# Optimization experiments

Hardware: AMD Instinct MI355X
Metric: run time of the kernel (lower is better)

## Reference

```python
import jax, jax.numpy as jnp
import numpy as np

DIM = 512          # must equal heads*dim_head for LayerNorm(dim) on q/k to be valid
SCALE = 64 ** -0.5  # dim_head ** -0.5
EPS = 1e-5


def layer_norm(x, g, b):
    mu = jnp.mean(x, axis=-1, keepdims=True)
    var = jnp.var(x, axis=-1, keepdims=True)
    return (x - mu) * jax.lax.rsqrt(var + EPS) * g + b


def setup_inputs() -> dict:
    key = jax.random.key(0)
    ks = jax.random.split(key, 8)
    b, n, m, d = 4, 4096, 4096, DIM
    x = jax.random.normal(ks[0], (b, n, d), dtype=jnp.float32)
    context = jax.random.normal(ks[1], (b, m, d), dtype=jnp.float32)
    s = 1.0 / np.sqrt(d)
    Wq = jax.random.normal(ks[2], (d, d), dtype=jnp.float32) * s
    Wkv = jax.random.normal(ks[3], (d, 2 * d), dtype=jnp.float32) * s
    Wo = jax.random.normal(ks[4], (d, d), dtype=jnp.float32) * s
    bo = jnp.zeros((d,), dtype=jnp.float32)
    ln_g = jnp.ones((d,), dtype=jnp.float32)
    ln_b = jnp.zeros((d,), dtype=jnp.float32)
    return {"x": x, "context": context, "Wq": Wq, "Wkv": Wkv, "Wo": Wo,
            "bo": bo, "ln_g": ln_g, "ln_b": ln_b}


def reference(x, context, Wq, Wkv, Wo, bo, ln_g, ln_b):
    # linear projections (no bias on q/kv, matching nn.Linear(bias=False))
    q = x @ Wq                                   # [b, n, d]
    kv = context @ Wkv                           # [b, m, 2d]
    k, v = jnp.split(kv, 2, axis=-1)             # [b, m, d] each
    # qk-norm: same LayerNorm params applied to q and k
    q = layer_norm(q, ln_g, ln_b)
    k = layer_norm(k, ln_g, ln_b)
    # NOTE: the original never splits heads -> full-dim single-head attention
    dots = jnp.einsum('bnd,bmd->bnm', q, k) * SCALE  # [b, n, m]
    attn = jax.nn.softmax(dots, axis=-1)
    out = jnp.einsum('bnm,bmd->bnd', attn, v)        # [b, n, d]
    return out @ Wo + bo
```

## Files before the change

kernel.cpp:

```cpp
#include <hip/hip_runtime.h>

typedef __bf16 bf16_t;
typedef bf16_t bf16x8 __attribute__((ext_vector_type(8)));
typedef float f32x4 __attribute__((ext_vector_type(4)));
typedef float f32x16 __attribute__((ext_vector_type(16)));

#define DIMD 512
#define NSEQ 4096
#define BATCH 4
#define ROWS (BATCH * NSEQ)
#define MPART 2
#define FIXMAX 20.0f

__device__ __forceinline__ void gload_lds16(const bf16_t* g, bf16_t* l) {
    __builtin_amdgcn_global_load_lds((const __attribute__((address_space(1))) unsigned int*)g,
                                     (__attribute__((address_space(3))) unsigned int*)l,
                                     16, 0, 0);
}

__device__ __forceinline__ int packbf(float lo, float hi) {
    union { bf16_t h[2]; int w; } u;
    u.h[0] = (bf16_t)lo;
    u.h[1] = (bf16_t)hi;
    return u.w;
}

__global__ void detect_mode(const unsigned* __restrict__ g, int* __restrict__ mode) {
    if (threadIdx.x == 0) *mode = (*g == 0x3F800000u) ? 1 : 0;
}

__global__ __launch_bounds__(256) void transpose_w(const void* __restrict__ in,
                                                   bf16_t* __restrict__ out,
                                                   int R, int C,
                                                   const int* __restrict__ modep) {
    int mode = *modep;
    int idx = blockIdx.x * 256 + threadIdx.x;
    if (idx < R * C) {
        int r = idx / C;
        int c = idx - r * C;
        float v = mode ? ((const float*)in)[idx] : (float)((const bf16_t*)in)[idx];
        out[c * R + r] = (bf16_t)v;
    }
}

__global__ void convert_vec(const void* __restrict__ in, bf16_t* __restrict__ out,
                            int n, const int* __restrict__ modep) {
    int mode = *modep;
    int i = blockIdx.x * 256 + threadIdx.x;
    if (i < n)
        out[i] = mode ? (bf16_t)((const float*)in)[i] : ((const bf16_t*)in)[i];
}

__global__ __launch_bounds__(256) void ln_rows(bf16_t* __restrict__ buf,
                                               const bf16_t* __restrict__ g,
                                               const bf16_t* __restrict__ bvec,
                                               float mult, int swz) {
    int w = threadIdx.x >> 6;
    int lane = threadIdx.x & 63;
    int row = blockIdx.x * 4 + w;
    const bf16_t* p = buf + (size_t)row * 512 + lane * 8;
    bf16x8 xv = *(const bf16x8*)p;
    float x[8];
    float s = 0.f, sq = 0.f;
#pragma unroll
    for (int i = 0; i < 8; ++i) {
        x[i] = (float)xv[i];
        s += x[i];
        sq += x[i] * x[i];
    }
#pragma unroll
    for (int off = 1; off < 64; off <<= 1) {
        s += __shfl_xor(s, off, 64);
        sq += __shfl_xor(sq, off, 64);
    }
    float mean = s * (1.0f / 512.0f);
    float var = fmaxf(sq * (1.0f / 512.0f) - mean * mean, 0.0f);
    float rstd = rsqrtf(var + 1e-5f);
    bf16x8 gv = *(const bf16x8*)(g + lane * 8);
    bf16x8 bv = *(const bf16x8*)(bvec + lane * 8);
    bf16x8 o;
#pragma unroll
    for (int i = 0; i < 8; ++i)
        o[i] = (bf16_t)(((x[i] - mean) * rstd * (float)gv[i] + (float)bv[i]) * mult);
    int outlane = swz ? (lane ^ (row & 7)) : lane;
    *(bf16x8*)(buf + (size_t)row * 512 + outlane * 8) = o;
}

template <int EPI>
__global__ __launch_bounds__(256) void gemm_nt(const void* __restrict__ A,
                                               const bf16_t* __restrict__ Bt,
                                               void* __restrict__ Cout,
                                               bf16_t* __restrict__ C2,
                                               int K, int ldc,
                                               const bf16_t* __restrict__ bias,
                                               const int* __restrict__ amodep,
                                               const int* __restrict__ omodep,
                                               const float* __restrict__ mlp) {
    __shared__ bf16_t As[128 * 32];
    __shared__ bf16_t Bs[128 * 32];
    int amode = (EPI != 2 && amodep) ? *amodep : 0;
    int t = threadIdx.x;
    int w = t >> 6;
    int lane = t & 63;
    int r16 = lane & 15;
    int quad = lane >> 4;
    int m0 = blockIdx.x * 128;
    int n0 = blockIdx.y * 128;
    int wr = w >> 1, wc = w & 1;

    f32x4 acc[4][4];
#pragma unroll
    for (int m = 0; m < 4; ++m)
#pragma unroll
        for (int n = 0; n < 4; ++n) acc[m][n] = f32x4{0.f, 0.f, 0.f, 0.f};

    int brow = w * 32 + (lane >> 2);
    int bswz = ((lane & 3) ^ ((brow >> 1) & 3)) * 8;
    const bf16_t* bsrc0 = Bt + (size_t)(n0 + brow) * K + bswz;
    const bf16_t* bsrc1 = bsrc0 + (size_t)16 * K;
    bf16_t* bdst0 = Bs + (w * 32) * 32;
    bf16_t* bdst1 = Bs + (w * 32 + 16) * 32;

    int a_r = t >> 1;
    int kh = (t & 1) * 16;
    int aswz = (a_r >> 1) & 3;
    bf16_t* adst0 = As + a_r * 32 + (((t & 1) * 2 + 0) ^ aswz) * 8;
    bf16_t* adst1 = As + a_r * 32 + (((t & 1) * 2 + 1) ^ aswz) * 8;

    float combine_scl = 0.f;
    if (EPI == 2)
        combine_scl = 1.0f / (mlp[m0 + a_r] + mlp[ROWS + m0 + a_r]);

    const bf16_t* abase = As + (wr * 64 + r16) * 32 + (quad ^ ((r16 >> 1) & 3)) * 8;
    const bf16_t* bbase = Bs + (wc * 64 + r16) * 32 + (quad ^ ((r16 >> 1) & 3)) * 8;

    for (int kt = 0; kt < K; kt += 32) {
        bf16x8 av0, av1;
        if (EPI == 2) {
            const bf16_t* r0 = (const bf16_t*)A + (size_t)(m0 + a_r) * 512 + kt + kh;
            const bf16_t* r1 = r0 + (size_t)ROWS * 512;
            bf16x8 x0 = *(const bf16x8*)r0;
            bf16x8 x1 = *(const bf16x8*)(r0 + 8);
            bf16x8 y0 = *(const bf16x8*)r1;
            bf16x8 y1 = *(const bf16x8*)(r1 + 8);
#pragma unroll
            for (int j = 0; j < 8; ++j) {
                av0[j] = (bf16_t)(((float)x0[j] + (float)y0[j]) * combine_scl);
                av1[j] = (bf16_t)(((float)x1[j] + (float)y1[j]) * combine_scl);
            }
        } else if (amode) {
            const float* Af = (const float*)A + (size_t)(m0 + a_r) * K + kt + kh;
            f32x4 f0 = *(const f32x4*)(Af + 0);
            f32x4 f1 = *(const f32x4*)(Af + 4);
            f32x4 f2 = *(const f32x4*)(Af + 8);
            f32x4 f3 = *(const f32x4*)(Af + 12);
#pragma unroll
            for (int j = 0; j < 4; ++j) {
                av0[j] = (bf16_t)f0[j];
                av0[j + 4] = (bf16_t)f1[j];
                av1[j] = (bf16_t)f2[j];
                av1[j + 4] = (bf16_t)f3[j];
            }
        } else {
            const bf16_t* Ab = (const bf16_t*)A + (size_t)(m0 + a_r) * K + kt + kh;
            av0 = *(const bf16x8*)Ab;
            av1 = *(const bf16x8*)(Ab + 8);
        }
        *(bf16x8*)adst0 = av0;
        *(bf16x8*)adst1 = av1;
        gload_lds16(bsrc0 + kt, bdst0);
        gload_lds16(bsrc1 + kt, bdst1);
        __syncthreads();

        bf16x8 af[4], bfr[4];
#pragma unroll
        for (int m = 0; m < 4; ++m) af[m] = *(const bf16x8*)(abase + m * 16 * 32);
#pragma unroll
        for (int n = 0; n < 4; ++n) bfr[n] = *(const bf16x8*)(bbase + n * 16 * 32);
        __builtin_amdgcn_s_setprio(1);
#pragma unroll
        for (int m = 0; m < 4; ++m)
#pragma unroll
            for (int n = 0; n < 4; ++n)
                acc[m][n] = __builtin_amdgcn_mfma_f32_16x16x32_bf16(af[m], bfr[n], acc[m][n], 0, 0, 0);
        __builtin_amdgcn_s_setprio(0);
        __syncthreads();
    }

    int omode = (EPI == 2 && omodep) ? *omodep : 0;
#pragma unroll
    for (int n = 0; n < 4; ++n) {
        int col = n0 + wc * 64 + n * 16 + r16;
        float bv = (EPI == 2 && bias) ? (float)bias[col] : 0.0f;
#pragma unroll
        for (int m = 0; m < 4; ++m) {
#pragma unroll
            for (int r = 0; r < 4; ++r) {
                int row = m0 + wr * 64 + m * 16 + quad * 4 + r;
                float val = acc[m][n][r] + bv;
                if (EPI == 0) {
                    ((bf16_t*)Cout)[(size_t)row * ldc + col] = (bf16_t)val;
                } else if (EPI == 1) {
                    if (col < 512) {
                        ((bf16_t*)Cout)[(size_t)row * 512 + col] = (bf16_t)val;
                    } else {
                        int d = col - 512;
                        C2[(size_t)(row >> 5) * 16384 + (d >> 3) * 256 + ((row & 31) >> 3) * 64
                           + (d & 7) * 8 + (row & 7)] = (bf16_t)val;
                    }
                } else {
                    if (omode)
                        ((float*)Cout)[(size_t)row * 512 + col] = val;
                    else
                        ((bf16_t*)Cout)[(size_t)row * 512 + col] = (bf16_t)val;
                }
            }
        }
    }
}

__global__ __launch_bounds__(512, 2) void flash_attn(const bf16_t* __restrict__ q,
                                                     const bf16_t* __restrict__ kn,
                                                     const bf16_t* __restrict__ vt,
                                                     bf16_t* __restrict__ Opart,
                                                     float* __restrict__ ml) {
    __shared__ bf16_t Ks[2][32 * 512];
    __shared__ bf16_t Vs[2][32 * 512];
    __shared__ float Pd[8][4][64][4];

    int t = threadIdx.x;
    int w = t >> 6;
    int lane = t & 63;
    int l31 = lane & 31;
    int h = lane >> 5;
    int qb = w & 3;
    int dh = w >> 2;
    int part = blockIdx.y;
    int qrow0 = blockIdx.x * 128 + qb * 32;
    int bb = (blockIdx.x * 128) >> 12;
    int krow0 = bb * NSEQ + part * (NSEQ / MPART);
    const int niter = (NSEQ / MPART) / 32;

    bf16x8 qf[16];
    {
        const bf16_t* qp = q + (size_t)(qrow0 + l31) * 512 + dh * 256 + h * 8;
#pragma unroll
        for (int ks = 0; ks < 16; ++ks) qf[ks] = *(const bf16x8*)(qp + ks * 16);
    }

    f32x16 O[8];
#pragma unroll
    for (int i = 0; i < 8; ++i)
#pragma unroll
        for (int j = 0; j < 16; ++j) O[i][j] = 0.f;
    float lsum = 0.f;
    int swz7 = l31 & 7;

    const bf16_t* KbA[2] = {&Ks[0][l31 * 512], &Ks[1][l31 * 512]};
    int voff = dh * 8192 + (l31 >> 3) * 256 + (l31 & 7) * 8 + h * 64;
    const bf16_t* VbA[2] = {&Vs[0][voff], &Vs[1][voff]};

#define STAGE(mt, bufi)                                                                          \
    {                                                                                            \
        if (w < 4) {                                                                             \
            const bf16_t* ksrc_ = kn + (size_t)(krow0 + (mt) + w * 8) * 512 + lane * 8;          \
            bf16_t* kd_ = &Ks[bufi][(w * 8) * 512];                                              \
            _Pragma("unroll")                                                                    \
            for (int i_ = 0; i_ < 8; ++i_)                                                       \
                gload_lds16(ksrc_ + i_ * 512, kd_ + i_ * 512);                                   \
        } else {                                                                                 \
            const bf16_t* vsrc_ = vt + (size_t)((krow0 + (mt)) >> 5) * 16384                     \
                                  + (size_t)((w - 4) * 8) * 512 + lane * 8;                      \
            bf16_t* vd_ = &Vs[bufi][((w - 4) * 8) * 512];                                        \
            _Pragma("unroll")                                                                    \
            for (int i_ = 0; i_ < 8; ++i_)                                                       \
                gload_lds16(vsrc_ + i_ * 512, vd_ + i_ * 512);                                   \
        }                                                                                        \
    }

#define FLASH_BODY(it, bufi)                                                                      \
    {                                                                                             \
        __syncthreads();                                                                          \
        if ((it) + 1 < niter) STAGE(((it) + 1) * 32, ((it) + 1) & 1);                             \
        f32x16 a;                                                                                 \
        _Pragma("unroll") for (int j = 0; j < 16; ++j) a[j] = 0.f;                                \
        __builtin_amdgcn_s_setprio(1);                                                            \
        _Pragma("unroll") for (int ks = 0; ks < 16; ++ks) {                                       \
            int fb = (dh * 32 + ks * 2 + h) ^ swz7;                                               \
            bf16x8 kf = *(const bf16x8*)(KbA[bufi] + fb * 8);                                     \
            a = __builtin_amdgcn_mfma_f32_32x32x16_bf16(kf, qf[ks], a, 0, 0, 0);                  \
        }                                                                                         \
        __builtin_amdgcn_s_setprio(0);                                                            \
        _Pragma("unroll") for (int c = 0; c < 4; ++c)                                             \
            *(f32x4*)&Pd[w][c][lane][0] = f32x4{a[4 * c], a[4 * c + 1], a[4 * c + 2], a[4 * c + 3]}; \
        asm volatile("s_waitcnt lgkmcnt(0)" ::: "memory");    \
        __builtin_amdgcn_s_barrier();                                                             \
        asm volatile("" ::: "memory");                                                            \
        float pr[16];                                                                             \
        float ls = 0.f;                                                                           \
        _Pragma("unroll") for (int c = 0; c < 4; ++c) {                                           \
            f32x4 pp = *(const f32x4*)&Pd[w ^ 4][c][lane][0];                                     \
            _Pragma("unroll") for (int j = 0; j < 4; ++j) {                                       \
                pr[4 * c + j] = __expf(a[4 * c + j] + pp[j] - FIXMAX);                            \
                ls += pr[4 * c + j];                                                              \
            }                                                                                     \
        }                                                                                         \
        lsum += ls;                                                                               \
        int pa0 = packbf(pr[0], pr[1]), pb0 = packbf(pr[4], pr[5]);                               \
        int pa1 = packbf(pr[2], pr[3]), pb1 = packbf(pr[6], pr[7]);                               \
        int pa2 = packbf(pr[8], pr[9]), pb2 = packbf(pr[12], pr[13]);                             \
        int pa3 = packbf(pr[10], pr[11]), pb3 = packbf(pr[14], pr[15]);                           \
        auto s0 = __builtin_amdgcn_permlane32_swap(pa0, pb0, false, false);                       \
        auto s1 = __builtin_amdgcn_permlane32_swap(pa1, pb1, false, false);                       \
        auto s2 = __builtin_amdgcn_permlane32_swap(pa2, pb2, false, false);                       \
        auto s3 = __builtin_amdgcn_permlane32_swap(pa3, pb3, false, false);                       \
        union { int w4[4]; bf16x8 v; } U0, U1;                                                    \
        U0.w4[0] = s0[0]; U0.w4[1] = s1[0]; U0.w4[2] = s0[1]; U0.w4[3] = s1[1];                   \
        U1.w4[0] = s2[0]; U1.w4[1] = s3[0]; U1.w4[2] = s2[1]; U1.w4[3] = s3[1];                   \
        bf16x8 pf0 = U0.v;                                     \
        bf16x8 pf1 = U1.v;                                     \
        __builtin_amdgcn_s_setprio(1);                                                            \
        _Pragma("unroll") for (int dt = 0; dt < 8; ++dt) {                                        \
            bf16x8 v0 = *(const bf16x8*)(VbA[bufi] + dt * 1024);                                  \
            bf16x8 v1 = *(const bf16x8*)(VbA[bufi] + dt * 1024 + 128);                            \
            O[dt] = __builtin_amdgcn_mfma_f32_32x32x16_bf16(pf0, v0, O[dt], 0, 0, 0);             \
            O[dt] = __builtin_amdgcn_mfma_f32_32x32x16_bf16(pf1, v1, O[dt], 0, 0, 0);             \
        }                                                                                         \
        __builtin_amdgcn_s_setprio(0);                                                            \
    }

    STAGE(0, 0);

    for (int it = 0; it < niter; it += 2) {
        FLASH_BODY(it, 0);
        FLASH_BODY(it + 1, 1);
    }

    lsum += __shfl_xor(lsum, 32, 64);
    if (dh == 0 && lane < 32) ml[(size_t)part * ROWS + qrow0 + l31] = lsum;
    bf16_t* op = Opart + (size_t)part * ROWS * 512;
#pragma unroll
    for (int dt = 0; dt < 8; ++dt)
#pragma unroll
        for (int r = 0; r < 16; ++r) {
            int qr = (r & 3) + 8 * (r >> 2) + 4 * h;
            op[(size_t)(qrow0 + qr) * 512 + dh * 256 + dt * 32 + l31] = (bf16_t)O[dt][r];
        }
#undef STAGE
#undef FLASH_BODY
}

extern "C" void kernel_launch(void* const* d_in, const int* in_sizes, int n_in,
                              void* d_out, int out_size, void* d_ws, size_t ws_size,
                              hipStream_t stream) {
    char* ws = (char*)d_ws;
    const size_t MB = 1024 * 1024;
    bf16_t* q     = (bf16_t*)(ws);
    bf16_t* kn    = (bf16_t*)(ws + 16 * MB);
    bf16_t* vt    = (bf16_t*)(ws + 32 * MB);
    bf16_t* Opart = (bf16_t*)(ws + 48 * MB);
    float*  mlbuf = (float*)(ws + 80 * MB);
    bf16_t* wqt   = (bf16_t*)(ws + 81 * MB);
    bf16_t* wkvt  = wqt + 512 * 512;
    bf16_t* wot   = wkvt + 512 * 1024;
    bf16_t* gq    = wot + 512 * 512;
    bf16_t* bb    = gq + 512;
    bf16_t* bob   = bb + 512;
    int* modep    = (int*)(bob + 512);

    detect_mode<<<1, 64, 0, stream>>>((const unsigned*)d_in[6], modep);

    transpose_w<<<1024, 256, 0, stream>>>(d_in[2], wqt, 512, 512, modep);
    transpose_w<<<2048, 256, 0, stream>>>(d_in[3], wkvt, 512, 1024, modep);
    transpose_w<<<1024, 256, 0, stream>>>(d_in[4], wot, 512, 512, modep);
    convert_vec<<<2, 256, 0, stream>>>(d_in[6], gq, 512, modep);
    convert_vec<<<2, 256, 0, stream>>>(d_in[7], bb, 512, modep);
    convert_vec<<<2, 256, 0, stream>>>(d_in[5], bob, 512, modep);

    gemm_nt<0><<<dim3(ROWS / 128, 4), 256, 0, stream>>>(d_in[0], wqt, q, nullptr, 512, 512, nullptr, modep, nullptr, nullptr);
    gemm_nt<1><<<dim3(ROWS / 128, 8), 256, 0, stream>>>(d_in[1], wkvt, kn, vt, 512, 0, nullptr, modep, nullptr, nullptr);

    ln_rows<<<dim3(ROWS / 4), 256, 0, stream>>>(q, gq, bb, 0.125f, 0);
    ln_rows<<<dim3(ROWS / 4), 256, 0, stream>>>(kn, gq, bb, 1.0f, 1);

    flash_attn<<<dim3(ROWS / 128, MPART), 512, 0, stream>>>(q, kn, vt, Opart, mlbuf);

    gemm_nt<2><<<dim3(ROWS / 128, 4), 256, 0, stream>>>(Opart, wot, d_out, nullptr, 512, 512, bob, nullptr, modep, mlbuf);
}
```

Measured before the change: 401.9 us.

## Merge prep kernels, retile GEMMs to 64x256, fuse Q layernorm into attention

Six weight/vector conversion kernels are merged into one prep launch, cutting launch overhead. The GEMM tile changes from 128x128 to 64x256, so each A row block is read once per 256 output columns and B is staged with four async loads per thread. The Q LayerNorm pass is removed and done inside flash_attn, which normalizes its 128 query rows into shared memory before loading fragments, saving a full read and write of q. The attention kernel now uses one flat shared-memory buffer reused for the Q staging and the K/V/P buffers, which costs an extra barrier and adds per-block LN work.

```diff
diff --git a/kernel.cpp b/kernel.cpp
--- a/kernel.cpp
+++ b/kernel.cpp
@@ -29,26 +29,41 @@
     if (threadIdx.x == 0) *mode = (*g == 0x3F800000u) ? 1 : 0;
 }
 
-__global__ __launch_bounds__(256) void transpose_w(const void* __restrict__ in,
-                                                   bf16_t* __restrict__ out,
-                                                   int R, int C,
-                                                   const int* __restrict__ modep) {
+__device__ __forceinline__ float cvt_in(const void* p, long i, int mode) {
+    return mode ? ((const float*)p)[i] : (float)((const bf16_t*)p)[i];
+}
+__global__ __launch_bounds__(256) void prep(const void* __restrict__ wq,
+                                            const void* __restrict__ wkv,
+                                            const void* __restrict__ wo,
+                                            const void* __restrict__ lng,
+                                            const void* __restrict__ lnb,
+                                            const void* __restrict__ bo,
+                                            bf16_t* __restrict__ wqt,
+                                            bf16_t* __restrict__ wkvt,
+                                            bf16_t* __restrict__ wot,
+                                            bf16_t* __restrict__ gq,
+                                            bf16_t* __restrict__ bb,
+                                            bf16_t* __restrict__ bob,
+                                            const int* __restrict__ modep) {
     int mode = *modep;
-    int idx = blockIdx.x * 256 + threadIdx.x;
-    if (idx < R * C) {
-        int r = idx / C;
-        int c = idx - r * C;
-        float v = mode ? ((const float*)in)[idx] : (float)((const bf16_t*)in)[idx];
-        out[c * R + r] = (bf16_t)v;
-    }
-}
-
-__global__ void convert_vec(const void* __restrict__ in, bf16_t* __restrict__ out,
-                            int n, const int* __restrict__ modep) {
-    int mode = *modep;
-    int i = blockIdx.x * 256 + threadIdx.x;
-    if (i < n)
-        out[i] = mode ? (bf16_t)((const float*)in)[i] : ((const bf16_t*)in)[i];
+    long idx = (long)blockIdx.x * 256 + threadIdx.x;
+    if (idx < 262144) {
+        int r = idx >> 9, c = idx & 511;
+        wqt[(long)c * 512 + r] = (bf16_t)cvt_in(wq, idx, mode);
+    } else if (idx < 262144 + 524288) {
+        long i = idx - 262144;
+        int r = i >> 10, c = i & 1023;
+        wkvt[(long)c * 512 + r] = (bf16_t)cvt_in(wkv, i, mode);
+    } else if (idx < 1048576) {
+        long i = idx - 786432;
+        int r = i >> 9, c = i & 511;
+        wot[(long)c * 512 + r] = (bf16_t)cvt_in(wo, i, mode);
+    } else {
+        long i = idx - 1048576;
+        if (i < 512) gq[i] = (bf16_t)cvt_in(lng, i, mode);
+        else if (i < 1024) bb[i - 512] = (bf16_t)cvt_in(lnb, i - 512, mode);
+        else if (i < 1536) bob[i - 1024] = (bf16_t)cvt_in(bo, i - 1024, mode);
+    }
 }
 
 __global__ __launch_bounds__(256) void ln_rows(bf16_t* __restrict__ buf,
@@ -96,92 +111,76 @@
                                                const int* __restrict__ amodep,
                                                const int* __restrict__ omodep,
                                                const float* __restrict__ mlp) {
-    __shared__ bf16_t As[128 * 32];
-    __shared__ bf16_t Bs[128 * 32];
+    __shared__ bf16_t As[64 * 32];
+    __shared__ bf16_t Bs[256 * 32];
     int amode = (EPI != 2 && amodep) ? *amodep : 0;
     int t = threadIdx.x;
     int w = t >> 6;
     int lane = t & 63;
     int r16 = lane & 15;
     int quad = lane >> 4;
-    int m0 = blockIdx.x * 128;
-    int n0 = blockIdx.y * 128;
+    int m0 = blockIdx.x * 64;
+    int n0 = blockIdx.y * 256;
     int wr = w >> 1, wc = w & 1;
 
-    f32x4 acc[4][4];
-#pragma unroll
-    for (int m = 0; m < 4; ++m)
-#pragma unroll
-        for (int n = 0; n < 4; ++n) acc[m][n] = f32x4{0.f, 0.f, 0.f, 0.f};
-
-    int brow = w * 32 + (lane >> 2);
+    f32x4 acc[2][8];
+#pragma unroll
+    for (int m = 0; m < 2; ++m)
+#pragma unroll
+        for (int n = 0; n < 8; ++n) acc[m][n] = f32x4{0.f, 0.f, 0.f, 0.f};
+
+    int brow = w * 64 + (lane >> 2);
     int bswz = ((lane & 3) ^ ((brow >> 1) & 3)) * 8;
-    const bf16_t* bsrc0 = Bt + (size_t)(n0 + brow) * K + bswz;
-    const bf16_t* bsrc1 = bsrc0 + (size_t)16 * K;
-    bf16_t* bdst0 = Bs + (w * 32) * 32;
-    bf16_t* bdst1 = Bs + (w * 32 + 16) * 32;
-
-    int a_r = t >> 1;
-    int kh = (t & 1) * 16;
-    int aswz = (a_r >> 1) & 3;
-    bf16_t* adst0 = As + a_r * 32 + (((t & 1) * 2 + 0) ^ aswz) * 8;
-    bf16_t* adst1 = As + a_r * 32 + (((t & 1) * 2 + 1) ^ aswz) * 8;
+    const bf16_t* bsrc = Bt + (size_t)(n0 + brow) * K + bswz;
+    bf16_t* bdst = Bs + (w * 64) * 32;
+
+    int a_r = t >> 2;
+    int ac = t & 3;
+    bf16_t* adst = As + a_r * 32 + (ac ^ ((a_r >> 1) & 3)) * 8;
 
     float combine_scl = 0.f;
     if (EPI == 2)
         combine_scl = 1.0f / (mlp[m0 + a_r] + mlp[ROWS + m0 + a_r]);
 
-    const bf16_t* abase = As + (wr * 64 + r16) * 32 + (quad ^ ((r16 >> 1) & 3)) * 8;
-    const bf16_t* bbase = Bs + (wc * 64 + r16) * 32 + (quad ^ ((r16 >> 1) & 3)) * 8;
+    int aswz = (r16 >> 1) & 3;
+    const bf16_t* abase = As + (wr * 32 + r16) * 32 + (quad ^ aswz) * 8;
+    const bf16_t* bbase = Bs + (wc * 128 + r16) * 32 + (quad ^ aswz) * 8;
 
     for (int kt = 0; kt < K; kt += 32) {
-        bf16x8 av0, av1;
+        bf16x8 av;
         if (EPI == 2) {
-            const bf16_t* r0 = (const bf16_t*)A + (size_t)(m0 + a_r) * 512 + kt + kh;
+            const bf16_t* r0 = (const bf16_t*)A + (size_t)(m0 + a_r) * 512 + kt + ac * 8;
             const bf16_t* r1 = r0 + (size_t)ROWS * 512;
             bf16x8 x0 = *(const bf16x8*)r0;
-            bf16x8 x1 = *(const bf16x8*)(r0 + 8);
             bf16x8 y0 = *(const bf16x8*)r1;
-            bf16x8 y1 = *(const bf16x8*)(r1 + 8);
-#pragma unroll
-            for (int j = 0; j < 8; ++j) {
-                av0[j] = (bf16_t)(((float)x0[j] + (float)y0[j]) * combine_scl);
-                av1[j] = (bf16_t)(((float)x1[j] + (float)y1[j]) * combine_scl);
-            }
+#pragma unroll
+            for (int j = 0; j < 8; ++j)
+                av[j] = (bf16_t)(((float)x0[j] + (float)y0[j]) * combine_scl);
         } else if (amode) {
-            const float* Af = (const float*)A + (size_t)(m0 + a_r) * K + kt + kh;
-            f32x4 f0 = *(const f32x4*)(Af + 0);
-            f32x4 f1 = *(const f32x4*)(Af + 4);
-            f32x4 f2 = *(const f32x4*)(Af + 8);
-            f32x4 f3 = *(const f32x4*)(Af + 12);
-#pragma unroll
-            for (int j = 0; j < 4; ++j) {
-                av0[j] = (bf16_t)f0[j];
-                av0[j + 4] = (bf16_t)f1[j];
-                av1[j] = (bf16_t)f2[j];
-                av1[j + 4] = (bf16_t)f3[j];
-            }
+            const float* Af = (const float*)A + (size_t)(m0 + a_r) * K + kt + ac * 8;
+            f32x4 lo = *(const f32x4*)Af;
+            f32x4 hi = *(const f32x4*)(Af + 4);
+#pragma unroll
+            for (int j = 0; j < 4; ++j) { av[j] = (bf16_t)lo[j]; av[j + 4] = (bf16_t)hi[j]; }
         } else {
-            const bf16_t* Ab = (const bf16_t*)A + (size_t)(m0 + a_r) * K + kt + kh;
-            av0 = *(const bf16x8*)Ab;
-            av1 = *(const bf16x8*)(Ab + 8);
+            av = *(const bf16x8*)((const bf16_t*)A + (size_t)(m0 + a_r) * K + kt + ac * 8);
         }
-        *(bf16x8*)adst0 = av0;
-        *(bf16x8*)adst1 = av1;
-        gload_lds16(bsrc0 + kt, bdst0);
-        gload_lds16(bsrc1 + kt, bdst1);
+        *(bf16x8*)adst = av;
+#pragma unroll
+        for (int k = 0; k < 4; ++k)
+            gload_lds16(bsrc + (size_t)(k * 16) * K + kt, bdst + (k * 16) * 32);
         __syncthreads();
 
-        bf16x8 af[4], bfr[4];
-#pragma unroll
-        for (int m = 0; m < 4; ++m) af[m] = *(const bf16x8*)(abase + m * 16 * 32);
-#pragma unroll
-        for (int n = 0; n < 4; ++n) bfr[n] = *(const bf16x8*)(bbase + n * 16 * 32);
+        bf16x8 af[2], bfr[8];
+#pragma unroll
+        for (int m = 0; m < 2; ++m) af[m] = *(const bf16x8*)(abase + m * 16 * 32);
+#pragma unroll
+        for (int n = 0; n < 8; ++n) bfr[n] = *(const bf16x8*)(bbase + n * 16 * 32);
         __builtin_amdgcn_s_setprio(1);
 #pragma unroll
-        for (int m = 0; m < 4; ++m)
-#pragma unroll
-            for (int n = 0; n < 4; ++n)
+        for (int m = 0; m < 2; ++m)
+#pragma unroll
+            for (int n = 0; n < 8; ++n)
                 acc[m][n] = __builtin_amdgcn_mfma_f32_16x16x32_bf16(af[m], bfr[n], acc[m][n], 0, 0, 0);
         __builtin_amdgcn_s_setprio(0);
         __syncthreads();
@@ -189,14 +188,14 @@
 
     int omode = (EPI == 2 && omodep) ? *omodep : 0;
 #pragma unroll
-    for (int n = 0; n < 4; ++n) {
-        int col = n0 + wc * 64 + n * 16 + r16;
+    for (int n = 0; n < 8; ++n) {
+        int col = n0 + wc * 128 + n * 16 + r16;
         float bv = (EPI == 2 && bias) ? (float)bias[col] : 0.0f;
 #pragma unroll
-        for (int m = 0; m < 4; ++m) {
+        for (int m = 0; m < 2; ++m) {
 #pragma unroll
             for (int r = 0; r < 4; ++r) {
-                int row = m0 + wr * 64 + m * 16 + quad * 4 + r;
+                int row = m0 + wr * 32 + m * 16 + quad * 4 + r;
                 float val = acc[m][n][r] + bv;
                 if (EPI == 0) {
                     ((bf16_t*)Cout)[(size_t)row * ldc + col] = (bf16_t)val;
@@ -223,10 +222,15 @@
                                                      const bf16_t* __restrict__ kn,
                                                      const bf16_t* __restrict__ vt,
                                                      bf16_t* __restrict__ Opart,
-                                                     float* __restrict__ ml) {
-    __shared__ bf16_t Ks[2][32 * 512];
-    __shared__ bf16_t Vs[2][32 * 512];
-    __shared__ float Pd[8][4][64][4];
+                                                     float* __restrict__ ml,
+                                                     const bf16_t* __restrict__ g,
+                                                     const bf16_t* __restrict__ bvec) {
+    __shared__ bf16_t SH[81920];
+    bf16_t* Ksb0 = SH;
+    bf16_t* Ksb1 = SH + 16384;
+    bf16_t* Vsb0 = SH + 32768;
+    bf16_t* Vsb1 = SH + 49152;
+    float* Pd = (float*)(SH + 65536);
 
     int t = threadIdx.x;
     int w = t >> 6;
@@ -241,12 +245,48 @@
     int krow0 = bb * NSEQ + part * (NSEQ / MPART);
     const int niter = (NSEQ / MPART) / 32;
 
+    {
+        int r8 = lane >> 3, c8 = lane & 7;
+#pragma unroll
+        for (int batch = 0; batch < 2; ++batch) {
+            int rloc = w * 16 + batch * 8 + r8;
+            const bf16_t* src = q + (size_t)(blockIdx.x * 128 + rloc) * 512 + c8 * 64;
+            bf16x8 xv[8];
+            float s = 0.f, sq = 0.f;
+#pragma unroll
+            for (int i = 0; i < 8; ++i) {
+                xv[i] = *(const bf16x8*)(src + i * 8);
+#pragma unroll
+                for (int j = 0; j < 8; ++j) { float f = (float)xv[i][j]; s += f; sq += f * f; }
+            }
+            s += __shfl_xor(s, 1, 64); sq += __shfl_xor(sq, 1, 64);
+            s += __shfl_xor(s, 2, 64); sq += __shfl_xor(sq, 2, 64);
+            s += __shfl_xor(s, 4, 64); sq += __shfl_xor(sq, 4, 64);
+            float mean = s * (1.0f / 512.0f);
+            float var = fmaxf(sq * (1.0f / 512.0f) - mean * mean, 0.0f);
+            float rstd = rsqrtf(var + 1e-5f);
+            bf16_t* dst = SH + rloc * 512 + c8 * 64;
+#pragma unroll
+            for (int i = 0; i < 8; ++i) {
+                bf16x8 gv = *(const bf16x8*)(g + c8 * 64 + i * 8);
+                bf16x8 bv = *(const bf16x8*)(bvec + c8 * 64 + i * 8);
+                bf16x8 o;
+#pragma unroll
+                for (int j = 0; j < 8; ++j)
+                    o[j] = (bf16_t)((((float)xv[i][j] - mean) * rstd * (float)gv[j] + (float)bv[j]) * 0.125f);
+                *(bf16x8*)(dst + i * 8) = o;
+            }
+        }
+    }
+    __syncthreads();
+
     bf16x8 qf[16];
     {
-        const bf16_t* qp = q + (size_t)(qrow0 + l31) * 512 + dh * 256 + h * 8;
+        const bf16_t* qp = SH + (size_t)(qb * 32 + l31) * 512 + dh * 256 + h * 8;
 #pragma unroll
         for (int ks = 0; ks < 16; ++ks) qf[ks] = *(const bf16x8*)(qp + ks * 16);
     }
+    __syncthreads();
 
     f32x16 O[8];
 #pragma unroll
@@ -256,22 +296,22 @@
     float lsum = 0.f;
     int swz7 = l31 & 7;
 
-    const bf16_t* KbA[2] = {&Ks[0][l31 * 512], &Ks[1][l31 * 512]};
+    const bf16_t* KbA[2] = {Ksb0 + l31 * 512, Ksb1 + l31 * 512};
     int voff = dh * 8192 + (l31 >> 3) * 256 + (l31 & 7) * 8 + h * 64;
-    const bf16_t* VbA[2] = {&Vs[0][voff], &Vs[1][voff]};
+    const bf16_t* VbA[2] = {Vsb0 + voff, Vsb1 + voff};
 
 #define STAGE(mt, bufi)                                                                          \
     {                                                                                            \
         if (w < 4) {                                                                             \
             const bf16_t* ksrc_ = kn + (size_t)(krow0 + (mt) + w * 8) * 512 + lane * 8;          \
-            bf16_t* kd_ = &Ks[bufi][(w * 8) * 512];                                              \
+            bf16_t* kd_ = ((bufi) ? Ksb1 : Ksb0) + (w * 8) * 512;                                \
             _Pragma("unroll")                                                                    \
             for (int i_ = 0; i_ < 8; ++i_)                                                       \
                 gload_lds16(ksrc_ + i_ * 512, kd_ + i_ * 512);                                   \
         } else {                                                                                 \
             const bf16_t* vsrc_ = vt + (size_t)((krow0 + (mt)) >> 5) * 16384                     \
                                   + (size_t)((w - 4) * 8) * 512 + lane * 8;                      \
-            bf16_t* vd_ = &Vs[bufi][((w - 4) * 8) * 512];                                        \
+            bf16_t* vd_ = ((bufi) ? Vsb1 : Vsb0) + ((w - 4) * 8) * 512;                          \
             _Pragma("unroll")                                                                    \
             for (int i_ = 0; i_ < 8; ++i_)                                                       \
                 gload_lds16(vsrc_ + i_ * 512, vd_ + i_ * 512);                                   \
@@ -292,14 +332,15 @@
         }                                                                                         \
         __builtin_amdgcn_s_setprio(0);                                                            \
         _Pragma("unroll") for (int c = 0; c < 4; ++c)                                             \
-            *(f32x4*)&Pd[w][c][lane][0] = f32x4{a[4 * c], a[4 * c + 1], a[4 * c + 2], a[4 * c + 3]}; \
+            *(f32x4*)(Pd + w * 1024 + c * 256 + lane * 4) =                                       \
+                f32x4{a[4 * c], a[4 * c + 1], a[4 * c + 2], a[4 * c + 3]};                        \
         asm volatile("s_waitcnt lgkmcnt(0)" ::: "memory");    \
         __builtin_amdgcn_s_barrier();                                                             \
         asm volatile("" ::: "memory");                                                            \
         float pr[16];                                                                             \
         float ls = 0.f;                                                                           \
         _Pragma("unroll") for (int c = 0; c < 4; ++c) {                                           \
-            f32x4 pp = *(const f32x4*)&Pd[w ^ 4][c][lane][0];                                     \
+            f32x4 pp = *(const f32x4*)(Pd + (w ^ 4) * 1024 + c * 256 + lane * 4);                 \
             _Pragma("unroll") for (int j = 0; j < 4; ++j) {                                       \
                 pr[4 * c + j] = __expf(a[4 * c + j] + pp[j] - FIXMAX);                            \
                 ls += pr[4 * c + j];                                                              \
@@ -370,20 +411,15 @@
 
     detect_mode<<<1, 64, 0, stream>>>((const unsigned*)d_in[6], modep);
 
-    transpose_w<<<1024, 256, 0, stream>>>(d_in[2], wqt, 512, 512, modep);
-    transpose_w<<<2048, 256, 0, stream>>>(d_in[3], wkvt, 512, 1024, modep);
-    transpose_w<<<1024, 256, 0, stream>>>(d_in[4], wot, 512, 512, modep);
-    convert_vec<<<2, 256, 0, stream>>>(d_in[6], gq, 512, modep);
-    convert_vec<<<2, 256, 0, stream>>>(d_in[7], bb, 512, modep);
-    convert_vec<<<2, 256, 0, stream>>>(d_in[5], bob, 512, modep);
-
-    gemm_nt<0><<<dim3(ROWS / 128, 4), 256, 0, stream>>>(d_in[0], wqt, q, nullptr, 512, 512, nullptr, modep, nullptr, nullptr);
-    gemm_nt<1><<<dim3(ROWS / 128, 8), 256, 0, stream>>>(d_in[1], wkvt, kn, vt, 512, 0, nullptr, modep, nullptr, nullptr);
-
-    ln_rows<<<dim3(ROWS / 4), 256, 0, stream>>>(q, gq, bb, 0.125f, 0);
+    prep<<<4102, 256, 0, stream>>>(d_in[2], d_in[3], d_in[4], d_in[6], d_in[7], d_in[5],
+                                   wqt, wkvt, wot, gq, bb, bob, modep);
+
+    gemm_nt<0><<<dim3(ROWS / 64, 2), 256, 0, stream>>>(d_in[0], wqt, q, nullptr, 512, 512, nullptr, modep, nullptr, nullptr);
+    gemm_nt<1><<<dim3(ROWS / 64, 4), 256, 0, stream>>>(d_in[1], wkvt, kn, vt, 512, 0, nullptr, modep, nullptr, nullptr);
+
     ln_rows<<<dim3(ROWS / 4), 256, 0, stream>>>(kn, gq, bb, 1.0f, 1);
 
-    flash_attn<<<dim3(ROWS / 128, MPART), 512, 0, stream>>>(q, kn, vt, Opart, mlbuf);
-
-    gemm_nt<2><<<dim3(ROWS / 128, 4), 256, 0, stream>>>(Opart, wot, d_out, nullptr, 512, 512, bob, nullptr, modep, mlbuf);
-}
+    flash_attn<<<dim3(ROWS / 128, MPART), 512, 0, stream>>>(q, kn, vt, Opart, mlbuf, gq, bb);
+
+    gemm_nt<2><<<dim3(ROWS / 64, 2), 256, 0, stream>>>(Opart, wot, d_out, nullptr, 512, 512, bob, nullptr, modep, mlbuf);
+}
```

Measured after the change: 386.3 us. 1.04x faster.
